# Kernel tuning notes

Hardware: AMD Instinct MI355X
Metric: run time of the kernel (lower is better)

The kernel has to match this reference:

```python
import jax, jax.numpy as jnp
import numpy as np

B, N, H, HEADS, L = 8, 64, 512, 8, 4
VOCAB, NBOND, CLS = 128, 8, 2
SP = H // HEADS
SCALE = float(np.sqrt(H))  # module divides by sqrt(hidden_dim), not sqrt(sp_dim)


def _ln(x):
    # fresh nn.LayerNorm each call -> gamma=1, beta=0
    m = jnp.mean(x, -1, keepdims=True)
    v = jnp.mean((x - m) ** 2, -1, keepdims=True)
    return (x - m) / jnp.sqrt(v + 1e-5)


def _split(x):  # [B,N,H] -> [B,h,N,sp]
    return x.reshape(B, N, HEADS, SP).transpose(0, 2, 1, 3)


def setup_inputs() -> dict:
    key = jax.random.key(0)
    ks = jax.random.split(key, 16)
    s = 0.05
    return {
        "input_batch": jax.random.randint(ks[0], (B, N), 0, VOCAB),
        "adj_m": jax.random.randint(ks[1], (B, N, N), 0, NBOND),
        "atom_emb": jax.random.normal(ks[2], (VOCAB, H), jnp.float32) * s,
        "bond_emb": jax.random.normal(ks[3], (NBOND, H), jnp.float32) * s,
        "Wq": jax.random.normal(ks[4], (L, H, H), jnp.float32) * s,
        "Wk": jax.random.normal(ks[5], (L, H, H), jnp.float32) * s,
        "Wv": jax.random.normal(ks[6], (L, H, H), jnp.float32) * s,
        "Wew": jax.random.normal(ks[7], (L, H, H), jnp.float32) * s,
        "Wstack": jax.random.normal(ks[8], (L, H, H), jnp.float32) * s,
        "Wf1": jax.random.normal(ks[9], (L, H, 4 * H), jnp.float32) * s,
        "Wf2": jax.random.normal(ks[10], (L, 4 * H, H), jnp.float32) * s,
        "Wout": jax.random.normal(ks[11], (H, H), jnp.float32) * s,
        "Wpred": jax.random.normal(ks[12], (H, CLS), jnp.float32) * s,
        "bpred": jnp.zeros((CLS,), jnp.float32),
    }


def _forward(input_batch, adj_m, atom_emb, bond_emb, Wq, Wk, Wv, Wew,
             Wstack, Wf1, Wf2, Wout, Wpred, bpred):
    x = atom_emb[input_batch]        # [B,N,H] atom embeddings
    bond = bond_emb[adj_m]           # [B,N,N,H] bond embeddings
    neg = jnp.where(adj_m > 0, 0.0, -jnp.inf)[:, None, :, :]  # [B,1,N,N]
    for l in range(L):
        xn = _ln(x)
        q = _split(xn @ Wq[l])
        k = _split(xn @ Wk[l])
        v = _split(xn @ Wv[l])
        ew = bond @ Wew[l]           # [B,N,N,H]
        w = ew.reshape(B, N, N, HEADS, SP).transpose(0, 3, 1, 2, 4)  # [B,h,N,N,sp]
        # bond_influence==1: sim_ij = q_i . (k_j + w_ij)
        logits = jnp.einsum('bhid,bhjd->bhij', q, k) \
               + jnp.einsum('bhid,bhijd->bhij', q, w)
        attn = jax.nn.softmax(logits / SCALE + neg, axis=-1)
        o = jnp.einsum('bhij,bhjd->bhid', attn, v)
        o = o.transpose(0, 2, 1, 3).reshape(B, N, H) @ Wstack[l]
        attn_resid = o + xn
        ff = jax.nn.relu(_ln(attn_resid) @ Wf1[l]) @ Wf2[l]
        x = ff + attn_resid          # transformer_output
        # edge attention update: softmax over {w.w, w.x_i, w.x_j}
        ew_s = jnp.sum(ew * ew, -1)                      # [B,N,N]
        a0 = jnp.einsum('bijh,bih->bij', ew, x)
        a1 = jnp.einsum('bijh,bjh->bij', ew, x)
        wgt = jax.nn.softmax(jnp.stack([ew_s, a0, a1], -1) / SCALE, -1)  # [B,N,N,3]
        bond = (wgt[..., 0:1] * ew
                + wgt[..., 1:2] * x[:, :, None, :]
                + wgt[..., 2:3] * x[:, None, :, :])      # new edge state
    cls = jnp.tanh(x[:, 0, :] @ Wout)
    return jax.nn.softmax(cls @ Wpred + bpred, axis=-1)


def reference(input_batch, adj_m, atom_emb, bond_emb, Wq, Wk, Wv, Wew,
              Wstack, Wf1, Wf2, Wout, Wpred, bpred):
    return _forward(input_batch, adj_m, atom_emb, bond_emb, Wq, Wk, Wv, Wew,
                    Wstack, Wf1, Wf2, Wout, Wpred, bpred)
```

## Files before the change

### kernel.cpp

```cpp
#include <hip/hip_runtime.h>
#include <hip/hip_bf16.h>

typedef __hip_bfloat16 bf16;

#define B_     8
#define N_     64
#define H_     512
#define HEADS_ 8
#define SP_    64
#define L_     4
static constexpr float INV_SCALE = 0.044194173824159216f;

typedef __attribute__((ext_vector_type(8))) short short8;
typedef __attribute__((ext_vector_type(4))) float f32x4;

__device__ __forceinline__ void unpack8(uint4 u, float* f) {
    f[0] = __uint_as_float(u.x << 16); f[1] = __uint_as_float(u.x & 0xffff0000u);
    f[2] = __uint_as_float(u.y << 16); f[3] = __uint_as_float(u.y & 0xffff0000u);
    f[4] = __uint_as_float(u.z << 16); f[5] = __uint_as_float(u.z & 0xffff0000u);
    f[6] = __uint_as_float(u.w << 16); f[7] = __uint_as_float(u.w & 0xffff0000u);
}

__device__ __forceinline__ bf16 f2bf(float v) { return __float2bfloat16(v); }

// ... 28 lines not shown
    const int cE = cA * 8;

    for (int k0 = kbeg; k0 < kend; k0 += 64) {
        uint4 a0 = *(const uint4*)(A  + (size_t)(bm + rA) * K + k0 + cE);
        uint4 a1 = *(const uint4*)(A  + (size_t)(bm + rA + 32) * K + k0 + cE);
        uint4 b0 = *(const uint4*)(Bt + (size_t)(bn + rA) * K + k0 + cE);
        uint4 b1 = *(const uint4*)(Bt + (size_t)(bn + rA + 32) * K + k0 + cE);
        __syncthreads();
        *(uint4*)(As + ksP * (64 * RSTR) + rA * RSTR + cB) = a0;
        *(uint4*)(As + ksP * (64 * RSTR) + (rA + 32) * RSTR + cB) = a1;
        *(uint4*)(Bs + ksP * (64 * RSTR) + rA * RSTR + cB) = b0;
        *(uint4*)(Bs + ksP * (64 * RSTR) + (rA + 32) * RSTR + cB) = b1;
        __syncthreads();
        short8 af[2][2], bfr[2][2];
        #pragma unroll
        for (int ks = 0; ks < 2; ++ks)
            #pragma unroll
            for (int t = 0; t < 2; ++t) {
                af[ks][t]  = *(const short8*)(As + ks * (64 * RSTR) + (wr + t * 16 + m0) * RSTR + q4 * 16);
                bfr[ks][t] = *(const short8*)(Bs + ks * (64 * RSTR) + (wc + t * 16 + m0) * RSTR + q4 * 16);
            }
        #pragma unroll
        for (int ks = 0; ks < 2; ++ks)
            #pragma unroll
            for (int mt = 0; mt < 2; ++mt)
                #pragma unroll
                for (int nt = 0; nt < 2; ++nt)
                    acc[mt][nt] = __builtin_amdgcn_mfma_f32_16x16x32_bf16(
                        af[ks][mt], bfr[ks][nt], acc[mt][nt], 0, 0, 0);
    }

    if (EPI <= 1) {
        float* C = (float*)Cv;
        #pragma unroll
        for (int mt = 0; mt < 2; ++mt)
            #pragma unroll
            for (int i = 0; i < 4; ++i) {
                int row = bm + wr + mt * 16 + q4 * 4 + i;
                #pragma unroll
                for (int nt = 0; nt < 2; ++nt) {
                    int col = bn + wc + nt * 16 + m0;
                    float v = acc[mt][nt][i];
                    if (EPI == 1) v += R[(size_t)row * N + col];
                    C[(size_t)row * N + col] = v;
                }
            }
    } else {
        bf16* C = (bf16*)Cv;
        #pragma unroll
        for (int mt = 0; mt < 2; ++mt)
            #pragma unroll
            for (int i = 0; i < 4; ++i) {
                int row = bm + wr + mt * 16 + q4 * 4 + i;
                #pragma unroll
                for (int nt = 0; nt < 2; ++nt) {
                    int col = bn + wc + nt * 16 + m0;
                    float v = acc[mt][nt][i];
                    if (EPI == 2) v = fmaxf(v, 0.0f);
                    C[(size_t)row * N + col] = __float2bfloat16(v);
                }
            }
    }
}

template <int EPI, bool SPLIT>
__launch_bounds__(256)
__global__ void mfma_gemm_s(const bf16* __restrict__ A, const bf16* __restrict__ Bt,
                            void* __restrict__ Cv, const float* __restrict__ R,
                            int M, int N, int K) {
    __shared__ __align__(16) char lds[4 * 64 * RSTR];
    int kbeg = 0, kend = K;
    const bf16* B2 = Bt;
    void* C2 = Cv;
    if (SPLIT) {
        int ks = K / gridDim.z;
        kbeg = blockIdx.z * ks;
        kend = kbeg + ks;
        C2 = (void*)((float*)Cv + (size_t)blockIdx.z * M * N);
        gemm64_body<0>(lds, A, B2, C2, nullptr, M, N, K, blockIdx.x, blockIdx.y, kbeg, kend);
    } else {
        B2 = Bt + (size_t)blockIdx.z * N * K;
        if (EPI <= 1) C2 = (void*)((float*)Cv + (size_t)blockIdx.z * M * N);
        gemm64_body<EPI>(lds, A, B2, C2, R, M, N, K, blockIdx.x, blockIdx.y, kbeg, kend);
    }
}


__device__ __forceinline__ void ptable_body(char* lds, const float* __restrict__ q,
        const bf16* __restrict__ Bt, float* __restrict__ P, int b, int h, bool shr) {
    char* As = lds;
    char* Bs = lds + 2 * 64 * RSTR;
    const int tid = threadIdx.x;
    const int w = tid >> 6, lane = tid & 63;
    const int wr = (w >> 1) * 32, wc = (w & 1) * 32;
    const int m0 = lane & 15, q4 = lane >> 4;
    const int rA = tid >> 3;
    const int cA = tid & 7;
    const int ksP = cA >> 2;
    const int cB = (cA & 3) * 16;
    const int cE = cA * 8;

    const float* Aq = q + (size_t)(b * 64) * 512 + h * 64;
    const bf16*  Bb = Bt + (shr ? (size_t)0 : (size_t)b * 64 * 512) + h * 64;

    float4 fa0 = *(const float4*)(Aq + (size_t)rA * 512 + cE);
    float4 fa1 = *(const float4*)(Aq + (size_t)rA * 512 + cE + 4);
    float4 fb0 = *(const float4*)(Aq + (size_t)(rA + 32) * 512 + cE);
    float4 fb1 = *(const float4*)(Aq + (size_t)(rA + 32) * 512 + cE + 4);
    uint4 bv0 = *(const uint4*)(Bb + (size_t)rA * 512 + cE);
    uint4 bv1 = *(const uint4*)(Bb + (size_t)(rA + 32) * 512 + cE);
    uint4 av0 = pack8bf(fa0, fa1);
    uint4 av1 = pack8bf(fb0, fb1);
    *(uint4*)(As + ksP * (64 * RSTR) + rA * RSTR + cB) = av0;
    *(uint4*)(As + ksP * (64 * RSTR) + (rA + 32) * RSTR + cB) = av1;
    *(uint4*)(Bs + ksP * (64 * RSTR) + rA * RSTR + cB) = bv0;
    *(uint4*)(Bs + ksP * (64 * RSTR) + (rA + 32) * RSTR + cB) = bv1;
    __syncthreads();

    f32x4 acc[2][2] = {};
    short8 af[2][2], bfr[2][2];
    #pragma unroll
    for (int ks = 0; ks < 2; ++ks)
        #pragma unroll
        for (int t = 0; t < 2; ++t) {
            af[ks][t]  = *(const short8*)(As + ks * (64 * RSTR) + (wr + t * 16 + m0) * RSTR + q4 * 16);
            bfr[ks][t] = *(const short8*)(Bs + ks * (64 * RSTR) + (wc + t * 16 + m0) * RSTR + q4 * 16);
        }
    #pragma unroll
    for (int ks = 0; ks < 2; ++ks)
        #pragma unroll
        for (int mt = 0; mt < 2; ++mt)
            #pragma unroll
            for (int nt = 0; nt < 2; ++nt)
                acc[mt][nt] = __builtin_amdgcn_mfma_f32_16x16x32_bf16(
                    af[ks][mt], bfr[ks][nt], acc[mt][nt], 0, 0, 0);

    #pragma unroll
    for (int mt = 0; mt < 2; ++mt)
        #pragma unroll
        for (int i = 0; i < 4; ++i) {
            int row = wr + mt * 16 + q4 * 4 + i;
            #pragma unroll
            for (int nt = 0; nt < 2; ++nt) {
                int col = wc + nt * 16 + m0;
                P[(((size_t)b * 8 + h) * 64 + row) * 64 + col] = acc[mt][nt][i];
            }
        }
}

__device__ __forceinline__ void ugemm_body(char* lds, const float* __restrict__ q,
        const bf16* __restrict__ wc3, bf16* __restrict__ ubf, int h, int mb, int nb) {
    char* As = lds;
    char* Bs = lds + 2 * 64 * RSTR;
    const int tid = threadIdx.x;
    const int w = tid >> 6, lane = tid & 63;
    const int wr = (w >> 1) * 32, wc = (w & 1) * 32;
    const int m0 = lane & 15, q4 = lane >> 4;
    const int rA = tid >> 3;
    const int cA = tid & 7;
    const int ksP = cA >> 2;
    const int cB = (cA & 3) * 16;
    const int cE = cA * 8;

    const float* Aq = q + (size_t)(mb * 64) * 512 + h * 64;
    const bf16*  Bt = wc3 + (size_t)(nb * 64) * 512 + h * 64;

// ... 41 lines not shown
            }
        }
}

__device__ __forceinline__ void coeff1_body(const int* __restrict__ adj,
        const float* __restrict__ c0a, const float* __restrict__ c1a, const float* __restrict__ c2a,
        const float* __restrict__ gbuf, int row, int j,
        float* __restrict__ w0o, float* __restrict__ w1o, float* __restrict__ w2o) {
    int b = row >> 6, i = row & 63;
    int p = row * 64 + j;
    int t = adj[p];
    const float* TXX = gbuf + 0 * 32768 + (size_t)b * 4096;
    const float* TEX = gbuf + 1 * 32768 + (size_t)b * 4096;
    const float* TXx = gbuf + 2 * 32768 + (size_t)b * 4096;
    const float* TEx = gbuf + 3 * 32768 + (size_t)b * 4096;
    const float* TEE = gbuf + 4 * 32768 + (size_t)b * 4096;
    float c0 = c0a[p], c1 = c1a[p], c2 = c2a[p];
    float s1 = c0 * TEx[t * 64 + i] + c1 * TXx[i * 64 + i] + c2 * TXx[j * 64 + i];
    float s2 = c0 * TEx[t * 64 + j] + c1 * TXx[i * 64 + j] + c2 * TXx[j * 64 + j];
    float s0 = c0 * c0 * TEE[t * 64 + t] + c1 * c1 * TXX[i * 64 + i] + c2 * c2 * TXX[j * 64 + j]
             + 2.f * c0 * c1 * TEX[t * 64 + i] + 2.f * c0 * c2 * TEX[t * 64 + j]
             + 2.f * c1 * c2 * TXX[i * 64 + j];
    float t0 = s0 * INV_SCALE, t1 = s1 * INV_SCALE, t2 = s2 * INV_SCALE;
    float m = fmaxf(t0, fmaxf(t1, t2));
    float e0 = expf(t0 - m), e1 = expf(t1 - m), e2 = expf(t2 - m);
    float inv = 1.0f / (e0 + e1 + e2);
    w0o[p] = e0 * inv;
    w1o[p] = e1 * inv;
    w2o[p] = e2 * inv;
}

__device__ __forceinline__ void coeff2_body(const int* __restrict__ adj,
        const float* __restrict__ c0a, const float* __restrict__ c1a, const float* __restrict__ c2a,
        const float* __restrict__ c0b, const float* __restrict__ c1b, const float* __restrict__ c2b,
        const float* __restrict__ gbuf, int row, int j,
        float* __restrict__ w0o, float* __restrict__ w1o, float* __restrict__ w2o) {
    int b = row >> 6, i = row & 63;
    int p = row * 64 + j;
    int t = adj[p];
    const float* TXX = gbuf + 0 * 32768 + (size_t)b * 4096;
    const float* TXY = gbuf + 1 * 32768 + (size_t)b * 4096;
    const float* TYY = gbuf + 2 * 32768 + (size_t)b * 4096;
    const float* TEX = gbuf + 3 * 32768 + (size_t)b * 4096;
    const float* TEY = gbuf + 4 * 32768 + (size_t)b * 4096;
    const float* TEE = gbuf + 5 * 32768 + (size_t)b * 4096;
    const float* TXx = gbuf + 6 * 32768 + (size_t)b * 4096;
    const float* TYx = gbuf + 7 * 32768 + (size_t)b * 4096;
    const float* TEx = gbuf + 8 * 32768 + (size_t)b * 4096;
    float a0 = c0b[p];
    float AE = a0 * c0a[p], Aa = a0 * c1a[p], Ab = a0 * c2a[p];
    float Ac = c1b[p], Ad = c2b[p];
    float s1 = AE * TEx[t * 64 + i] + Aa * TXx[i * 64 + i] + Ab * TXx[j * 64 + i]
             + Ac * TYx[i * 64 + i] + Ad * TYx[j * 64 + i];
    float s2 = AE * TEx[t * 64 + j] + Aa * TXx[i * 64 + j] + Ab * TXx[j * 64 + j]
             + Ac * TYx[i * 64 + j] + Ad * TYx[j * 64 + j];
    float s0 = AE * AE * TEE[t * 64 + t] + Aa * Aa * TXX[i * 64 + i] + Ab * Ab * TXX[j * 64 + j]
             + Ac * Ac * TYY[i * 64 + i] + Ad * Ad * TYY[j * 64 + j]
             + 2.f * AE * Aa * TEX[t * 64 + i] + 2.f * AE * Ab * TEX[t * 64 + j]
             + 2.f * AE * Ac * TEY[t * 64 + i] + 2.f * AE * Ad * TEY[t * 64 + j]
             + 2.f * Aa * Ab * TXX[i * 64 + j]
             + 2.f * Aa * Ac * TXY[i * 64 + i] + 2.f * Aa * Ad * TXY[i * 64 + j]
             + 2.f * Ab * Ac * TXY[j * 64 + i] + 2.f * Ab * Ad * TXY[j * 64 + j]
             + 2.f * Ac * Ad * TYY[i * 64 + j];
    float t0 = s0 * INV_SCALE, t1 = s1 * INV_SCALE, t2 = s2 * INV_SCALE;
    float m = fmaxf(t0, fmaxf(t1, t2));
    float e0 = expf(t0 - m), e1 = expf(t1 - m), e2 = expf(t2 - m);
    float inv = 1.0f / (e0 + e1 + e2);
    w0o[p] = e0 * inv;
    w1o[p] = e1 * inv;
    w2o[p] = e2 * inv;
}

__launch_bounds__(256)
__global__ void setup_kernel(const int* __restrict__ ids, const float* __restrict__ atom_emb,
                             const float* __restrict__ bond_emb,
                             const float* __restrict__ Wq, const float* __restrict__ Wk,
                             const float* __restrict__ Wv, const float* __restrict__ Wew,
                             const float* __restrict__ Wst,
                             const float* __restrict__ Wf1, const float* __restrict__ Wf2,
                             float* __restrict__ xn, bf16* __restrict__ xn_bf,
                             bf16* __restrict__ qkvt, bf16* __restrict__ ewt,
                             bf16* __restrict__ stackt,
                             bf16* __restrict__ f1t, bf16* __restrict__ f2t,
                             bf16* __restrict__ bond_bf, bf16* __restrict__ wc3) {
    __shared__ __align__(16) float smem[64 * 65];
    const size_t KN = (size_t)H_ * H_;
    int bid = blockIdx.x;
    int tid = threadIdx.x;

    if (bid < 512) {
        int row = bid;
        const float* r = atom_emb + (size_t)ids[row] * H_;
        float x0 = r[tid], x1 = r[tid + 256];
        float s = x0 + x1, sq = x0 * x0 + x1 * x1;
        #pragma unroll
        for (int off = 32; off; off >>= 1) {
            s  += __shfl_xor(s,  off);
            sq += __shfl_xor(sq, off);
        }
        int w = tid >> 6;
        if ((tid & 63) == 0) { smem[w] = s; smem[4 + w] = sq; }
        __syncthreads();
        float S = smem[0] + smem[1] + smem[2] + smem[3];
        float Q = smem[4] + smem[5] + smem[6] + smem[7];
        float mean = S * (1.0f / H_);
        float var  = Q * (1.0f / H_) - mean * mean;
        float inv  = rsqrtf(var + 1e-5f);
        float y0 = (x0 - mean) * inv, y1 = (x1 - mean) * inv;
        xn[(size_t)row * H_ + tid]       = y0;
        xn[(size_t)row * H_ + tid + 256] = y1;
        xn_bf[(size_t)row * H_ + tid]       = f2bf(y0);
        xn_bf[(size_t)row * H_ + tid + 256] = f2bf(y1);
    } else if (bid < 3840) {
        const float* W; bf16* Wt; int K, N, kb, nb;
        if (bid < 1792) {
            int idx = bid - 512;
            int z = idx >> 6, rem = idx & 63;
            kb = rem & 7; nb = rem >> 3;
            K = 512; N = 512;
            if (z < 12) {
                int sss = z >> 2, l = z & 3;
                W  = (sss == 0 ? Wq : sss == 1 ? Wk : Wv) + (size_t)l * KN;
                Wt = qkvt + (size_t)l * 3 * KN + (size_t)sss * KN;
            } else if (z < 16) {
                int l = z - 12;
                W = Wew + (size_t)l * KN; Wt = ewt + (size_t)l * KN;
            } else {
                int l = z - 16;
                W = Wst + (size_t)l * KN; Wt = stackt + (size_t)l * KN;
            }
        } else {
            int idx = bid - 1792;
            int z = idx >> 8;
            int idx2 = idx & 255;
            const size_t KN4 = (size_t)4 * H_ * H_;
            if (z < 4) {
                W = Wf1 + (size_t)z * KN4; Wt = f1t + (size_t)z * KN4; K = 512; N = 2048;
                kb = idx2 & 7; nb = idx2 >> 3;
            } else {
                W = Wf2 + (size_t)(z - 4) * KN4; Wt = f2t + (size_t)(z - 4) * KN4; K = 2048; N = 512;
                kb = idx2 >> 3; nb = idx2 & 7;
            }
        }
        int k0 = kb * 64, n0 = nb * 64;
        float (*tt)[65] = (float(*)[65])smem;
        int rr = tid >> 4, c4 = (tid & 15) * 4;
        #pragma unroll
        for (int it = 0; it < 4; ++it) {
            float4 v = *(const float4*)(W + (size_t)(k0 + rr + it * 16) * N + n0 + c4);
            tt[rr + it * 16][c4 + 0] = v.x;
            tt[rr + it * 16][c4 + 1] = v.y;
            tt[rr + it * 16][c4 + 2] = v.z;
            tt[rr + it * 16][c4 + 3] = v.w;
        }
        __syncthreads();
        int nr = tid >> 3, k8 = (tid & 7) * 8;
        #pragma unroll
        for (int it = 0; it < 2; ++it) {
            int nn = nr + it * 32;
            __align__(16) bf16 ob[8];
            #pragma unroll
            for (int e = 0; e < 8; ++e)
                ob[e] = f2bf(tt[k8 + e][nn]);
            *(uint4*)(Wt + (size_t)(n0 + nn) * K + k0 + k8) = *(const uint4*)ob;
        }
    } else if (bid < 3968) {
        int idx = bid - 3840;
        int t = idx >> 1;
        int c = (idx & 1) * 256 + tid;
        bond_bf[t * 512 + c] = (t < 8) ? f2bf(bond_emb[t * 512 + c]) : f2bf(0.0f);
    } else {
        int idx = bid - 3968;
        int gid = idx * 256 + tid;
// ... 171 lines not shown
    ptable_body(lds, q, Bt, P, b, h, z == 1);
}

__launch_bounds__(256)
__global__ void l3qkv_g2(const bf16* __restrict__ xn_bf, const bf16* __restrict__ qkvt_l,
                         float* __restrict__ qkv,
                         const bf16* __restrict__ xw12, const bf16* __restrict__ x2w2,
                         const bf16* __restrict__ e0w12, const bf16* __restrict__ x_bf,
                         float* __restrict__ gbuf) {
    __shared__ __align__(16) char lds[4 * 64 * RSTR];
    int bid = blockIdx.x;
    if (bid < 192) {
        int z = bid >> 6, rem = bid & 63;
        int mb = rem >> 3, by = rem & 7;
        gemm64_body<0>(lds, xn_bf, qkvt_l + (size_t)z * 262144,
                       qkv + (size_t)z * 262144, nullptr, 512, 512, 512, mb, by, 0, 512);
    } else {
        int k = bid - 192;
        int b = k & 7, z = k >> 3;
        size_t ob = (size_t)b * 32768;
        const bf16 *A, *Bt;
        switch (z) {
            case 0: A = xw12 + ob; Bt = xw12 + ob; break;
            case 1: A = xw12 + ob; Bt = x2w2 + ob; break;
            case 2: A = x2w2 + ob; Bt = x2w2 + ob; break;
            case 3: A = e0w12;     Bt = xw12 + ob; break;
            case 4: A = e0w12;     Bt = x2w2 + ob; break;
            case 5: A = e0w12;     Bt = e0w12;     break;
            case 6: A = xw12 + ob; Bt = x_bf + ob; break;
            case 7: A = x2w2 + ob; Bt = x_bf + ob; break;
            default: A = e0w12;    Bt = x_bf + ob; break;
        }
        float* C = gbuf + (size_t)z * 32768 + (size_t)b * 4096;
        gemm64_body<0>(lds, A, Bt, C, nullptr, 64, 64, 512, 0, 0, 0, 512);
    }
}

__launch_bounds__(256)
__global__ void u_c2(const float* __restrict__ q, const bf16* __restrict__ wc3,
                     bf16* __restrict__ ubf,
                     const int* __restrict__ adj,
                     const float* __restrict__ c0a, const float* __restrict__ c1a,
                     const float* __restrict__ c2a,
                     const float* __restrict__ c0b, const float* __restrict__ c1b,
                     const float* __restrict__ c2b,
                     const float* __restrict__ gbuf,
                     float* __restrict__ w0o, float* __restrict__ w1o,
                     float* __restrict__ w2o) {
    __shared__ __align__(16) char lds[4 * 64 * RSTR];
    int bid = blockIdx.x;
    if (bid < 512) {
        int h = bid >> 6, mb = (bid >> 3) & 7, nb = bid & 7;
        ugemm_body(lds, q, wc3, ubf, h, mb, nb);
    } else {
        int k = bid - 512;
        int tid = threadIdx.x;
        int j = tid & 63;
        #pragma unroll
        for (int pass = 0; pass < 2; ++pass) {
            int row = k * 8 + pass * 4 + (tid >> 6);
            coeff2_body(adj, c0a, c1a, c2a, c0b, c1b, c2b, gbuf, row, j, w0o, w1o, w2o);
        }
    }
}

__launch_bounds__(256)
__global__ void mbuf_gemm(const bf16* __restrict__ ubf, const bf16* __restrict__ xw12,
                          const bf16* __restrict__ x2w2, const bf16* __restrict__ x_bf,
                          const bf16* __restrict__ e0w12,
                          float* __restrict__ MX, float* __restrict__ MY,
                          float* __restrict__ MZ, float* __restrict__ DE) {
    __shared__ __align__(16) char lds[4 * 64 * RSTR];
    int b = blockIdx.x, mt = blockIdx.y, z = blockIdx.z;
    const bf16* A = ubf + (size_t)b * 512 * 512;
    const bf16* Bt;
    float* C;
    if (z == 0)      { Bt = xw12 + (size_t)b * 64 * 512; C = MX + (size_t)b * 512 * 64; }
    else if (z == 1) { Bt = x2w2 + (size_t)b * 64 * 512; C = MY + (size_t)b * 512 * 64; }
    else if (z == 2) { Bt = x_bf + (size_t)b * 64 * 512; C = MZ + (size_t)b * 512 * 64; }
    else             { Bt = e0w12;                        C = DE + (size_t)b * 512 * 64; }
    gemm64_body<0>(lds, A, Bt, C, nullptr, 512, 64, 512, mt, 0, 0, 512);
}

__global__ void reduce_stack_ln(const float* __restrict__ part, const float* __restrict__ base,
                                float* __restrict__ resid, bf16* __restrict__ ffin_bf) {
    const int MN = 512 * H_;
    int row = blockIdx.x;
    int tid = threadIdx.x;
    size_t b0 = (size_t)row * H_;
    float v0 = base[b0 + tid], v1 = base[b0 + tid + 256];
    #pragma unroll
    for (int s = 0; s < 4; ++s) {
        v0 += part[(size_t)s * MN + b0 + tid];
        v1 += part[(size_t)s * MN + b0 + tid + 256];
    }
    resid[b0 + tid] = v0;
    resid[b0 + tid + 256] = v1;
    float s = v0 + v1, sq = v0 * v0 + v1 * v1;
    #pragma unroll
    for (int off = 32; off; off >>= 1) {
        s  += __shfl_xor(s,  off);
        sq += __shfl_xor(sq, off);
    }
    __shared__ float ls[4], lq[4];
    int w = tid >> 6;
    if ((tid & 63) == 0) { ls[w] = s; lq[w] = sq; }
    __syncthreads();
    float S = ls[0] + ls[1] + ls[2] + ls[3];
    float Q = lq[0] + lq[1] + lq[2] + lq[3];
    float mean = S * (1.0f / H_);
    float var  = Q * (1.0f / H_) - mean * mean;
    float inv  = rsqrtf(var + 1e-5f);
    ffin_bf[b0 + tid]       = f2bf((v0 - mean) * inv);
    ffin_bf[b0 + tid + 256] = f2bf((v1 - mean) * inv);
}

template <bool DO_LN>
__global__ void reduce_ln_kernel(const float* __restrict__ part, const float* __restrict__ resid,
                                 float* __restrict__ x, bf16* __restrict__ x_bf,
                                 float* __restrict__ xn, bf16* __restrict__ xn_bf) {
    const int MN = 512 * H_;
    int row = blockIdx.x;
    int tid = threadIdx.x;
    size_t base = (size_t)row * H_;
    float v0 = resid[base + tid], v1 = resid[base + tid + 256];
    #pragma unroll
    for (int s = 0; s < 4; ++s) {
        v0 += part[(size_t)s * MN + base + tid];
        v1 += part[(size_t)s * MN + base + tid + 256];
    }
    x[base + tid] = v0;
    x[base + tid + 256] = v1;
    x_bf[base + tid]       = f2bf(v0);
    x_bf[base + tid + 256] = f2bf(v1);
    if (DO_LN) {
        float s = v0 + v1, sq = v0 * v0 + v1 * v1;
        #pragma unroll
        for (int off = 32; off; off >>= 1) {
            s  += __shfl_xor(s,  off);
            sq += __shfl_xor(sq, off);
        }
        __shared__ float ls[4], lq[4];
        int w = tid >> 6;
        if ((tid & 63) == 0) { ls[w] = s; lq[w] = sq; }
        __syncthreads();
        float S = ls[0] + ls[1] + ls[2] + ls[3];
        float Q = lq[0] + lq[1] + lq[2] + lq[3];
        float mean = S * (1.0f / H_);
        float var  = Q * (1.0f / H_) - mean * mean;
        float inv  = rsqrtf(var + 1e-5f);
        float y0 = (v0 - mean) * inv, y1 = (v1 - mean) * inv;
        xn[base + tid]       = y0;
        xn[base + tid + 256] = y1;
        xn_bf[base + tid]       = f2bf(y0);
        xn_bf[base + tid + 256] = f2bf(y1);
    }
}

template <bool GATHER>
__global__ void attn_kernel(const float* __restrict__ qkv, const bf16* __restrict__ ew,
                            const int* __restrict__ adj, bf16* __restrict__ o) {
    const float* q = qkv;
    const float* k = qkv + (size_t)512 * H_;
    const float* v = qkv + (size_t)1024 * H_;
    int bi = blockIdx.x;
    int b  = bi >> 6;
    int ty = threadIdx.y;
    int h  = blockIdx.y * 4 + ty;
    int lane = threadIdx.x;
    __shared__ float qs[4][64], as[4][64];
    qs[ty][lane] = q[(size_t)bi * H_ + h * 64 + lane];
    __syncthreads();

    int j = lane;
    int pair = bi * 64 + j;
    int aj = adj[pair];
    const float4* k4 = (const float4*)(k + (size_t)(b * 64 + j) * H_ + h * 64);
    const uint4*  w4 = (const uint4*)((GATHER ? ew + (size_t)aj * H_
                                              : ew + (size_t)pair * H_) + h * 64);
    float acc = 0.f;
    #pragma unroll
    for (int t = 0; t < 8; ++t) {
        uint4 wu = w4[t];
        float4 ka = k4[2 * t], kb = k4[2 * t + 1];
        float wf[8];
        unpack8(wu, wf);
        const float* qq = &qs[ty][t * 8];
        acc += qq[0] * (ka.x + wf[0]) + qq[1] * (ka.y + wf[1])
             + qq[2] * (ka.z + wf[2]) + qq[3] * (ka.w + wf[3])
             + qq[4] * (kb.x + wf[4]) + qq[5] * (kb.y + wf[5])
             + qq[6] * (kb.z + wf[6]) + qq[7] * (kb.w + wf[7]);
    }
    float logit = acc * INV_SCALE;
    if (aj <= 0) logit = -INFINITY;

    float m = logit;
    #pragma unroll
    for (int off = 32; off; off >>= 1) m = fmaxf(m, __shfl_xor(m, off));
    float p = expf(logit - m);
    float s = p;
    #pragma unroll
    for (int off = 32; off; off >>= 1) s += __shfl_xor(s, off);
    as[ty][lane] = p / s;
    __syncthreads();

    const float* vbase = v + (size_t)(b * 64) * H_ + h * 64;
    float oacc = 0.f;
    int d = lane;
    #pragma unroll 8
    for (int jj = 0; jj < 64; ++jj)
        oacc += as[ty][jj] * vbase[(size_t)jj * H_ + d];
    o[(size_t)bi * H_ + h * 64 + d] = __float2bfloat16(oacc);
}

template <int MODE>
__global__ void attn13_kernel(const float* __restrict__ qkv, const int* __restrict__ adj,
        const float* __restrict__ c0a, const float* __restrict__ c1a, const float* __restrict__ c2a,
        const float* __restrict__ c0b, const float* __restrict__ c1b, const float* __restrict__ c2b,
        const float* __restrict__ PX, const float* __restrict__ PY, const float* __restrict__ PE,
        bf16* __restrict__ o) {
    const float* q = qkv;
    const float* k = qkv + (size_t)512 * H_;
    const float* v = qkv + (size_t)1024 * H_;
    int bi = blockIdx.x;
    int b  = bi >> 6, i = bi & 63;
    int ty = threadIdx.y;
    int h  = blockIdx.y * 4 + ty;
    int lane = threadIdx.x;
    __shared__ float qs[4][64], as[4][64];
    qs[ty][lane] = q[(size_t)bi * H_ + h * 64 + lane];
    __syncthreads();

    int j = lane;
    int p = bi * 64 + j;
    int t = adj[p];
    size_t pb = (((size_t)b * 8 + h) * 64 + i) * 64;
    float acc;
    if (MODE == 1) {
        acc = c0a[p] * PE[pb + t] + c1a[p] * PX[pb + i] + c2a[p] * PX[pb + j];
    } else {
        float a0 = c0b[p];
// ... 14 lines not shown
    if (t <= 0) logit = -INFINITY;

    float m = logit;
    #pragma unroll
    for (int off = 32; off; off >>= 1) m = fmaxf(m, __shfl_xor(m, off));
    float pe = expf(logit - m);
    float s = pe;
    #pragma unroll
    for (int off = 32; off; off >>= 1) s += __shfl_xor(s, off);
    as[ty][lane] = pe / s;
    __syncthreads();

    const float* vbase = v + (size_t)(b * 64) * H_ + h * 64;
    float oacc = 0.f;
    int d = lane;
    #pragma unroll 8
    for (int jj = 0; jj < 64; ++jj)
        oacc += as[ty][jj] * vbase[(size_t)jj * H_ + d];
    o[(size_t)bi * H_ + h * 64 + d] = __float2bfloat16(oacc);
}

__global__ void attn3s2_kernel(const float* __restrict__ qkv, const int* __restrict__ adj,
        const float* __restrict__ c0a, const float* __restrict__ c1a, const float* __restrict__ c2a,
        const float* __restrict__ c0b, const float* __restrict__ c1b, const float* __restrict__ c2b,
        const float* __restrict__ v0c, const float* __restrict__ v1c, const float* __restrict__ v2c,
        const float* __restrict__ MX, const float* __restrict__ MY,
        const float* __restrict__ MZ, const float* __restrict__ DE,
        bf16* __restrict__ o) {
    const float* q = qkv;
    const float* k = qkv + (size_t)512 * H_;
    const float* v = qkv + (size_t)1024 * H_;
    int bi = blockIdx.x;
    int b  = bi >> 6, i = bi & 63;
    int ty = threadIdx.y;
    int h  = blockIdx.y * 4 + ty;
    int lane = threadIdx.x;
    __shared__ float qs[4][64], as[4][64];
    qs[ty][lane] = q[(size_t)bi * H_ + h * 64 + lane];
    __syncthreads();

    int j = lane;
    int p = bi * 64 + j;
    int t = adj[p];
    float v0 = v0c[p];
    float q0 = v0 * c0b[p];
    float AE = q0 * c0a[p], Aa = q0 * c1a[p], Ab = q0 * c2a[p];
    float Ac = v0 * c1b[p], Ad = v0 * c2b[p];
    float Ae = v1c[p], Af = v2c[p];
    size_t rb = ((size_t)b * 512 + i * 8 + h) * 64;
    float acc = AE * DE[rb + t]
              + Aa * MX[rb + i] + Ac * MY[rb + i] + Ae * MZ[rb + i]
              + Ab * MX[rb + j] + Ad * MY[rb + j] + Af * MZ[rb + j];

    const float4* k4 = (const float4*)(k + (size_t)(b * 64 + j) * H_ + h * 64);
    #pragma unroll
    for (int tt = 0; tt < 8; ++tt) {
        float4 ka = k4[2 * tt], kb = k4[2 * tt + 1];
        const float* qq = &qs[ty][tt * 8];
        acc += qq[0] * ka.x + qq[1] * ka.y + qq[2] * ka.z + qq[3] * ka.w
             + qq[4] * kb.x + qq[5] * kb.y + qq[6] * kb.z + qq[7] * kb.w;
    }
    float logit = acc * INV_SCALE;
    if (t <= 0) logit = -INFINITY;

    float m = logit;
    #pragma unroll
    for (int off = 32; off; off >>= 1) m = fmaxf(m, __shfl_xor(m, off));
    float pe = expf(logit - m);
    float s = pe;
    #pragma unroll
    for (int off = 32; off; off >>= 1) s += __shfl_xor(s, off);
    as[ty][lane] = pe / s;
    __syncthreads();

    const float* vbase = v + (size_t)(b * 64) * H_ + h * 64;
    float oacc = 0.f;
    int d = lane;
    #pragma unroll 8
    for (int jj = 0; jj < 64; ++jj)
        oacc += as[ty][jj] * vbase[(size_t)jj * H_ + d];
    o[(size_t)bi * H_ + h * 64 + d] = __float2bfloat16(oacc);
}

__global__ void cls_part_kernel(const float* __restrict__ x, const float* __restrict__ Wout,
                                float* __restrict__ clspart) {
    int b  = blockIdx.x;
    int cb = blockIdx.y;
    int ks = blockIdx.z;
    int tid = threadIdx.x;
    int c  = cb * 64 + (tid & 63);
    int kk = tid >> 6;
    const float* xr = x + (size_t)(b * 64) * H_;
    int h0 = ks * 128 + kk * 32;
    float acc = 0.f;
    #pragma unroll
    for (int h = 0; h < 32; ++h)
        acc += xr[h0 + h] * Wout[(size_t)(h0 + h) * H_ + c];
    __shared__ float red[4][64];
    red[kk][tid & 63] = acc;
    __syncthreads();
    if (tid < 64) {
        float v = red[0][tid] + red[1][tid] + red[2][tid] + red[3][tid];
        clspart[((size_t)ks * 8 + b) * H_ + cb * 64 + tid] = v;
    }
}

__global__ void cls_pred2_kernel(const float* __restrict__ clspart,
                                 const float* __restrict__ Wpred,
                                 const float* __restrict__ bpred,
                                 float* __restrict__ out) {
    int b = blockIdx.x;
    int tid = threadIdx.x;
    __shared__ float red0[4], red1[4];
    float a0 = 0.f, a1 = 0.f;
    #pragma unroll
    for (int t = 0; t < 2; ++t) {
        int c = tid + t * 256;
        float v = clspart[((size_t)0 * 8 + b) * H_ + c]
                + clspart[((size_t)1 * 8 + b) * H_ + c]
                + clspart[((size_t)2 * 8 + b) * H_ + c]
                + clspart[((size_t)3 * 8 + b) * H_ + c];
        float tv = tanhf(v);
        a0 += tv * Wpred[c * 2 + 0];
        a1 += tv * Wpred[c * 2 + 1];
    }
    #pragma unroll
    for (int off = 32; off; off >>= 1) {
        a0 += __shfl_xor(a0, off);
        a1 += __shfl_xor(a1, off);
    }
    int w = tid >> 6;
    if ((tid & 63) == 0) { red0[w] = a0; red1[w] = a1; }
    __syncthreads();
    if (tid == 0) {
        float s0 = red0[0] + red0[1] + red0[2] + red0[3] + bpred[0];
        float s1 = red1[0] + red1[1] + red1[2] + red1[3] + bpred[1];
        float m = fmaxf(s0, s1);
        float e0 = expf(s0 - m), e1 = expf(s1 - m);
        float inv = 1.0f / (e0 + e1);
        out[b * 2 + 0] = e0 * inv;
        out[b * 2 + 1] = e1 * inv;
    }
}

extern "C" void kernel_launch(void* const* d_in, const int* in_sizes, int n_in,
                              void* d_out, int out_size, void* d_ws, size_t ws_size,
                              hipStream_t stream) {
    const int*   ids      = (const int*)d_in[0];
    const int*   adj      = (const int*)d_in[1];
    const float* atom_emb = (const float*)d_in[2];
    const float* bond_emb = (const float*)d_in[3];
    const float* Wq     = (const float*)d_in[4];
    const float* Wk     = (const float*)d_in[5];
    const float* Wv     = (const float*)d_in[6];
    const float* Wew    = (const float*)d_in[7];
    const float* Wstack = (const float*)d_in[8];
    const float* Wf1    = (const float*)d_in[9];
    const float* Wf2    = (const float*)d_in[10];
    const float* Wout   = (const float*)d_in[11];
    const float* Wpred  = (const float*)d_in[12];
    const float* bpred  = (const float*)d_in[13];

    char* ws = (char*)d_ws;
    size_t off = 0;
    auto alloc = [&](size_t bytes) {
        size_t o = off;
        off += (bytes + 255) & ~(size_t)255;
        return o;
    };
    const size_t ROWS  = (size_t)B_ * N_;
    const size_t PAIRS = (size_t)B_ * N_ * N_;
    const size_t KN    = (size_t)H_ * H_;

    float* x       = (float*)(ws + alloc(ROWS * H_ * 4));
    float* xn      = (float*)(ws + alloc(ROWS * H_ * 4));
    bf16*  xn_bf   = (bf16*) (ws + alloc(ROWS * H_ * 2));
    bf16*  x_bf    = (bf16*) (ws + alloc(ROWS * H_ * 2));
    float* qkv     = (float*)(ws + alloc(3 * ROWS * H_ * 4));
    bf16*  o_bf    = (bf16*) (ws + alloc(ROWS * H_ * 2));
    float* resid   = (float*)(ws + alloc(ROWS * H_ * 4));
    bf16*  ffin_bf = (bf16*) (ws + alloc(ROWS * H_ * 2));
    bf16*  ffh_bf  = (bf16*) (ws + alloc(ROWS * 4 * H_ * 2));
    float* part    = (float*)(ws + alloc(4 * ROWS * H_ * 4));
    float* clspart = (float*)(ws + alloc(4 * 8 * H_ * 4));
    bf16*  ubf     = (bf16*) (ws + alloc(ROWS * 8 * 512 * 2));
    float* MX      = (float*)(ws + alloc((size_t)4096 * 64 * 4));
    float* MY      = (float*)(ws + alloc((size_t)4096 * 64 * 4));
    float* MZ      = (float*)(ws + alloc((size_t)4096 * 64 * 4));
    float* DE      = (float*)(ws + alloc((size_t)4096 * 64 * 4));
    float* PT0     = (float*)(ws + alloc((size_t)4096 * 64 * 4));
    float* PT1     = (float*)(ws + alloc((size_t)4096 * 64 * 4));
    float* PT2     = (float*)(ws + alloc((size_t)4096 * 64 * 4));
    float* gbuf    = (float*)(ws + alloc((size_t)9 * 8 * 4096 * 4));
    bf16*  wc3     = (bf16*) (ws + alloc(KN * 2));
    bf16*  bond_bf = (bf16*) (ws + alloc(64 * H_ * 2));
    bf16*  E0      = (bf16*) (ws + alloc(64 * H_ * 2));
    bf16*  e0w1    = (bf16*) (ws + alloc(64 * H_ * 2));
    bf16*  e0w12   = (bf16*) (ws + alloc(64 * H_ * 2));
    bf16*  xw1     = (bf16*) (ws + alloc(KN * 2));
    bf16*  xw12    = (bf16*) (ws + alloc(KN * 2));
    bf16*  x2w2    = (bf16*) (ws + alloc(KN * 2));
    float* cw      = (float*)(ws + alloc(9 * PAIRS * 4));
    bf16*  qkvt    = (bf16*) (ws + alloc((size_t)L_ * 3 * KN * 2));
    bf16*  ewt     = (bf16*) (ws + alloc((size_t)L_ * KN * 2));
    bf16*  stackt  = (bf16*) (ws + alloc((size_t)L_ * KN * 2));
    bf16*  f1t     = (bf16*) (ws + alloc((size_t)L_ * 4 * KN * 2));
    bf16*  f2t     = (bf16*) (ws + alloc((size_t)L_ * 4 * KN * 2));
    (void)ws_size;

    float* cw0a = cw;
    float* cw1a = cw + PAIRS;
    float* cw2a = cw + 2 * PAIRS;
    float* cw0b = cw + 3 * PAIRS;
    float* cw1b = cw + 4 * PAIRS;
    float* cw2b = cw + 5 * PAIRS;
    float* cw0c = cw + 6 * PAIRS;
    float* cw1c = cw + 7 * PAIRS;
    float* cw2c = cw + 8 * PAIRS;

    setup_kernel<<<4096, 256, 0, stream>>>(ids, atom_emb, bond_emb,
                                           Wq, Wk, Wv, Wew, Wstack, Wf1, Wf2,
                                           xn, xn_bf, qkvt, ewt, stackt, f1t, f2t,
                                           bond_bf, wc3);

    for (int l = 0; l < L_; ++l) {
        if (l == 0) {
            qkv0_e0<<<200, 256, 0, stream>>>(xn_bf, qkvt, qkv, bond_bf, ewt, E0);
            attn_kernel<true><<<dim3(512, 2), dim3(64, 4), 0, stream>>>(qkv, E0, adj, o_bf);
        } else if (l == 1) {
            basis1_qkv_ec<<<2312, 256, 0, stream>>>(
                x_bf, E0, ewt + KN, xw1, e0w1, xn_bf, qkvt + (size_t)3 * KN, qkv,
                adj, x, cw0a, cw1a, cw2a);
            ptable_kernel<<<dim3(8, 8, 2), 256, 0, stream>>>(qkv, xw1, e0w1, PT0, PT1);
            attn13_kernel<1><<<dim3(512, 2), dim3(64, 4), 0, stream>>>(
                qkv, adj, cw0a, cw1a, cw2a, nullptr, nullptr, nullptr,
                PT0, nullptr, PT1, o_bf);
        } else if (l == 2) {
            basis2_qkv_g1<<<368, 256, 0, stream>>>(
                xw1, x_bf, e0w1, ewt + 2 * KN, xw12, x2w2, e0w12,
                xn_bf, qkvt + (size_t)6 * KN, qkv, gbuf);
            ptable2c<<<256, 256, 0, stream>>>(
                qkv, xw12, x2w2, e0w12, PT0, PT1, PT2,
                adj, cw0a, cw1a, cw2a, gbuf, cw0b, cw1b, cw2b);
            attn13_kernel<2><<<dim3(512, 2), dim3(64, 4), 0, stream>>>(
                qkv, adj, cw0a, cw1a, cw2a, cw0b, cw1b, cw2b,
                PT0, PT1, PT2, o_bf);
        } else {
            l3qkv_g2<<<264, 256, 0, stream>>>(
                xn_bf, qkvt + (size_t)9 * KN, qkv, xw12, x2w2, e0w12, x_bf, gbuf);
            u_c2<<<576, 256, 0, stream>>>(
                qkv, wc3, ubf, adj, cw0a, cw1a, cw2a, cw0b, cw1b, cw2b,
                gbuf, cw0c, cw1c, cw2c);
            mbuf_gemm<<<dim3(8, 8, 4), 256, 0, stream>>>(ubf, xw12, x2w2, x_bf, e0w12,
                                                         MX, MY, MZ, DE);
            attn3s2_kernel<<<dim3(512, 2), dim3(64, 4), 0, stream>>>(
                qkv, adj, cw0a, cw1a, cw2a, cw0b, cw1b, cw2b, cw0c, cw1c, cw2c,
                MX, MY, MZ, DE, o_bf);
        }

        mfma_gemm_s<0, true><<<dim3(8, 8, 4), 256, 0, stream>>>(
            o_bf, stackt + (size_t)l * KN, part, nullptr, 512, 512, 512);
        reduce_stack_ln<<<512, 256, 0, stream>>>(part, xn, resid, ffin_bf);
        mfma_gemm_s<2, false><<<dim3(8, 32), 256, 0, stream>>>(
            ffin_bf, f1t + (size_t)l * 4 * KN, ffh_bf, nullptr, 512, 2048, 512);
        mfma_gemm_s<0, true><<<dim3(8, 8, 4), 256, 0, stream>>>(
            ffh_bf, f2t + (size_t)l * 4 * KN, part, nullptr, 512, 512, 2048);
        if (l < L_ - 1)
            reduce_ln_kernel<true><<<512, 256, 0, stream>>>(part, resid, x, x_bf, xn, xn_bf);
        else
            reduce_ln_kernel<false><<<512, 256, 0, stream>>>(part, resid, x, x_bf, xn, xn_bf);
    }

    cls_part_kernel<<<dim3(8, 8, 4), 256, 0, stream>>>(x, Wout, clspart);
    cls_pred2_kernel<<<8, 256, 0, stream>>>(clspart, Wpred, bpred, (float*)d_out);
}
```

Before: 345.9 us.

## Fuse split-K reductions and LayerNorm into GEMM tails via last-block atomic counters

The split-K Wstack and Wf2 GEMMs now do their own reduction and LayerNorm. An atomic counter per 64-row stripe picks the last block to finish, and that block sums the four partials and applies the residual and LN, so the separate reduce kernels are gone. The two classifier kernels are merged the same way, with one last block computing the tanh, pred and softmax. This removes about nine kernel launches and their launch gaps, at the cost of serialising the reduction of each stripe onto a single block and adding fence and atomic overhead.

Result: slower. 691.1 us (+99.8%).

```diff
diff --git a/kernel.cpp b/kernel.cpp
--- a/kernel.cpp
+++ b/kernel.cpp
@@ -134,6 +134,108 @@
         B2 = Bt + (size_t)blockIdx.z * N * K;
         if (EPI <= 1) C2 = (void*)((float*)Cv + (size_t)blockIdx.z * M * N);
         gemm64_body<EPI>(lds, A, B2, C2, R, M, N, K, blockIdx.x, blockIdx.y, kbeg, kend);
+    }
+}
+
+__launch_bounds__(256)
+__global__ void stackred_kernel(const bf16* __restrict__ o_bf, const bf16* __restrict__ stackt_l,
+                                float* __restrict__ part, const float* __restrict__ xn,
+                                float* __restrict__ resid, bf16* __restrict__ ffin_bf,
+                                int* __restrict__ cnt) {
+    __shared__ __align__(16) char lds[4 * 64 * RSTR];
+    __shared__ int lastf;
+    int bid = blockIdx.x;
+    int bz = bid >> 6, rem = bid & 63, bx = rem >> 3, by = rem & 7;
+    gemm64_body<0>(lds, o_bf, stackt_l, part + (size_t)bz * 262144, nullptr,
+                   512, 512, 512, bx, by, bz * 128, bz * 128 + 128);
+    __threadfence();
+    __syncthreads();
+    if (threadIdx.x == 0) lastf = (atomicAdd(&cnt[bx], 1) == 31);
+    __syncthreads();
+    if (!lastf) return;
+    __threadfence();
+    const int MN = 512 * 512;
+    int wv = threadIdx.x >> 6, lane = threadIdx.x & 63;
+    for (int k = 0; k < 16; ++k) {
+        int r = bx * 64 + wv * 16 + k;
+        size_t rb = (size_t)r * 512;
+        float vals[8], s = 0.f, sq = 0.f;
+        #pragma unroll
+        for (int e = 0; e < 8; ++e) {
+            int col = lane + e * 64;
+            float v = xn[rb + col] + part[0 * MN + rb + col] + part[1 * MN + rb + col]
+                    + part[2 * MN + rb + col] + part[3 * MN + rb + col];
+            vals[e] = v; s += v; sq += v * v;
+            resid[rb + col] = v;
+        }
+        #pragma unroll
+        for (int off = 32; off; off >>= 1) {
+            s  += __shfl_xor(s,  off);
+            sq += __shfl_xor(sq, off);
+        }
+        float mean = s * (1.0f / H_);
+        float var  = sq * (1.0f / H_) - mean * mean;
+        float inv  = rsqrtf(var + 1e-5f);
+        #pragma unroll
+        for (int e = 0; e < 8; ++e) {
+            int col = lane + e * 64;
+            ffin_bf[rb + col] = f2bf((vals[e] - mean) * inv);
+        }
+    }
+}
+
+template <bool DO_LN>
+__launch_bounds__(256)
+__global__ void ff2red_kernel(const bf16* __restrict__ ffh_bf, const bf16* __restrict__ f2t_l,
+                              float* __restrict__ part, const float* __restrict__ resid,
+                              float* __restrict__ x, bf16* __restrict__ x_bf,
+                              float* __restrict__ xn, bf16* __restrict__ xn_bf,
+                              int* __restrict__ cnt) {
+    __shared__ __align__(16) char lds[4 * 64 * RSTR];
+    __shared__ int lastf;
+    int bid = blockIdx.x;
+    int bz = bid >> 6, rem = bid & 63, bx = rem >> 3, by = rem & 7;
+    gemm64_body<0>(lds, ffh_bf, f2t_l, part + (size_t)bz * 262144, nullptr,
+                   512, 512, 2048, bx, by, bz * 512, bz * 512 + 512);
+    __threadfence();
+    __syncthreads();
+    if (threadIdx.x == 0) lastf = (atomicAdd(&cnt[bx], 1) == 31);
+    __syncthreads();
+    if (!lastf) return;
+    __threadfence();
+    const int MN = 512 * 512;
+    int wv = threadIdx.x >> 6, lane = threadIdx.x & 63;
+    for (int k = 0; k < 16; ++k) {
+        int r = bx * 64 + wv * 16 + k;
+        size_t rb = (size_t)r * 512;
+        float vals[8], s = 0.f, sq = 0.f;
+        #pragma unroll
+        for (int e = 0; e < 8; ++e) {
+            int col = lane + e * 64;
+            float v = resid[rb + col] + part[0 * MN + rb + col] + part[1 * MN + rb + col]
+                    + part[2 * MN + rb + col] + part[3 * MN + rb + col];
+            vals[e] = v;
+            if (DO_LN) { s += v; sq += v * v; }
+            x[rb + col] = v;
+            x_bf[rb + col] = f2bf(v);
+        }
+        if (DO_LN) {
+            #pragma unroll
+            for (int off = 32; off; off >>= 1) {
+                s  += __shfl_xor(s,  off);
+                sq += __shfl_xor(sq, off);
+            }
+            float mean = s * (1.0f / H_);
+            float var  = sq * (1.0f / H_) - mean * mean;
+            float inv  = rsqrtf(var + 1e-5f);
+            #pragma unroll
+            for (int e = 0; e < 8; ++e) {
+                int col = lane + e * 64;
+                float y = (vals[e] - mean) * inv;
+                xn[rb + col] = y;
+                xn_bf[rb + col] = f2bf(y);
+            }
+        }
     }
 }
 
@@ -341,13 +443,15 @@
                              bf16* __restrict__ qkvt, bf16* __restrict__ ewt,
                              bf16* __restrict__ stackt,
                              bf16* __restrict__ f1t, bf16* __restrict__ f2t,
-                             bf16* __restrict__ bond_bf, bf16* __restrict__ wc3) {
+                             bf16* __restrict__ bond_bf, bf16* __restrict__ wc3,
+                             int* __restrict__ cnt) {
     __shared__ __align__(16) float smem[64 * 65];
     const size_t KN = (size_t)H_ * H_;
     int bid = blockIdx.x;
     int tid = threadIdx.x;
 
     if (bid < 512) {
+        if (bid == 0 && tid < 72) cnt[tid] = 0;
         int row = bid;
         const float* r = atom_emb + (size_t)ids[row] * H_;
         float x0 = r[tid], x1 = r[tid + 256];
@@ -685,81 +789,6 @@
     gemm64_body<0>(lds, A, Bt, C, nullptr, 512, 64, 512, mt, 0, 0, 512);
 }
 
-__global__ void reduce_stack_ln(const float* __restrict__ part, const float* __restrict__ base,
-                                float* __restrict__ resid, bf16* __restrict__ ffin_bf) {
-    const int MN = 512 * H_;
-    int row = blockIdx.x;
-    int tid = threadIdx.x;
-    size_t b0 = (size_t)row * H_;
-    float v0 = base[b0 + tid], v1 = base[b0 + tid + 256];
-    #pragma unroll
-    for (int s = 0; s < 4; ++s) {
-        v0 += part[(size_t)s * MN + b0 + tid];
-        v1 += part[(size_t)s * MN + b0 + tid + 256];
-    }
-    resid[b0 + tid] = v0;
-    resid[b0 + tid + 256] = v1;
-    float s = v0 + v1, sq = v0 * v0 + v1 * v1;
-    #pragma unroll
-    for (int off = 32; off; off >>= 1) {
-        s  += __shfl_xor(s,  off);
-        sq += __shfl_xor(sq, off);
-    }
-    __shared__ float ls[4], lq[4];
-    int w = tid >> 6;
-    if ((tid & 63) == 0) { ls[w] = s; lq[w] = sq; }
-    __syncthreads();
-    float S = ls[0] + ls[1] + ls[2] + ls[3];
-    float Q = lq[0] + lq[1] + lq[2] + lq[3];
-    float mean = S * (1.0f / H_);
-    float var  = Q * (1.0f / H_) - mean * mean;
-    float inv  = rsqrtf(var + 1e-5f);
-    ffin_bf[b0 + tid]       = f2bf((v0 - mean) * inv);
-    ffin_bf[b0 + tid + 256] = f2bf((v1 - mean) * inv);
-}
-
-template <bool DO_LN>
-__global__ void reduce_ln_kernel(const float* __restrict__ part, const float* __restrict__ resid,
-                                 float* __restrict__ x, bf16* __restrict__ x_bf,
-                                 float* __restrict__ xn, bf16* __restrict__ xn_bf) {
-    const int MN = 512 * H_;
-    int row = blockIdx.x;
-    int tid = threadIdx.x;
-    size_t base = (size_t)row * H_;
-    float v0 = resid[base + tid], v1 = resid[base + tid + 256];
-    #pragma unroll
-    for (int s = 0; s < 4; ++s) {
-        v0 += part[(size_t)s * MN + base + tid];
-        v1 += part[(size_t)s * MN + base + tid + 256];
-    }
-    x[base + tid] = v0;
-    x[base + tid + 256] = v1;
-    x_bf[base + tid]       = f2bf(v0);
-    x_bf[base + tid + 256] = f2bf(v1);
-    if (DO_LN) {
-        float s = v0 + v1, sq = v0 * v0 + v1 * v1;
-        #pragma unroll
-        for (int off = 32; off; off >>= 1) {
-            s  += __shfl_xor(s,  off);
-            sq += __shfl_xor(sq, off);
-        }
-        __shared__ float ls[4], lq[4];
-        int w = tid >> 6;
-        if ((tid & 63) == 0) { ls[w] = s; lq[w] = sq; }
-        __syncthreads();
-        float S = ls[0] + ls[1] + ls[2] + ls[3];
-        float Q = lq[0] + lq[1] + lq[2] + lq[3];
-        float mean = S * (1.0f / H_);
-        float var  = Q * (1.0f / H_) - mean * mean;
-        float inv  = rsqrtf(var + 1e-5f);
-        float y0 = (v0 - mean) * inv, y1 = (v1 - mean) * inv;
-        xn[base + tid]       = y0;
-        xn[base + tid + 256] = y1;
-        xn_bf[base + tid]       = f2bf(y0);
-        xn_bf[base + tid + 256] = f2bf(y1);
-    }
-}
-
 template <bool GATHER>
 __global__ void attn_kernel(const float* __restrict__ qkv, const bf16* __restrict__ ew,
                             const int* __restrict__ adj, bf16* __restrict__ o) {
@@ -940,11 +969,13 @@
     o[(size_t)bi * H_ + h * 64 + d] = __float2bfloat16(oacc);
 }
 
-__global__ void cls_part_kernel(const float* __restrict__ x, const float* __restrict__ Wout,
-                                float* __restrict__ clspart) {
-    int b  = blockIdx.x;
-    int cb = blockIdx.y;
-    int ks = blockIdx.z;
+__launch_bounds__(256)
+__global__ void cls_kernel(const float* __restrict__ x, const float* __restrict__ Wout,
+                           float* __restrict__ clspart,
+                           const float* __restrict__ Wpred, const float* __restrict__ bpred,
+                           float* __restrict__ out, int* __restrict__ cnt) {
+    int bid = blockIdx.x;
+    int ks = bid & 3, cb = (bid >> 2) & 7, b = bid >> 5;
     int tid = threadIdx.x;
     int c  = cb * 64 + (tid & 63);
     int kk = tid >> 6;
@@ -961,43 +992,46 @@
         float v = red[0][tid] + red[1][tid] + red[2][tid] + red[3][tid];
         clspart[((size_t)ks * 8 + b) * H_ + cb * 64 + tid] = v;
     }
-}
-
-__global__ void cls_pred2_kernel(const float* __restrict__ clspart,
-                                 const float* __restrict__ Wpred,
-                                 const float* __restrict__ bpred,
-                                 float* __restrict__ out) {
-    int b = blockIdx.x;
-    int tid = threadIdx.x;
+    __threadfence();
+    __syncthreads();
+    __shared__ int lastf;
+    if (tid == 0) lastf = (atomicAdd(&cnt[0], 1) == 255);
+    __syncthreads();
+    if (!lastf) return;
+    __threadfence();
+
     __shared__ float red0[4], red1[4];
-    float a0 = 0.f, a1 = 0.f;
-    #pragma unroll
-    for (int t = 0; t < 2; ++t) {
-        int c = tid + t * 256;
-        float v = clspart[((size_t)0 * 8 + b) * H_ + c]
-                + clspart[((size_t)1 * 8 + b) * H_ + c]
-                + clspart[((size_t)2 * 8 + b) * H_ + c]
-                + clspart[((size_t)3 * 8 + b) * H_ + c];
-        float tv = tanhf(v);
-        a0 += tv * Wpred[c * 2 + 0];
-        a1 += tv * Wpred[c * 2 + 1];
-    }
-    #pragma unroll
-    for (int off = 32; off; off >>= 1) {
-        a0 += __shfl_xor(a0, off);
-        a1 += __shfl_xor(a1, off);
-    }
-    int w = tid >> 6;
-    if ((tid & 63) == 0) { red0[w] = a0; red1[w] = a1; }
-    __syncthreads();
-    if (tid == 0) {
-        float s0 = red0[0] + red0[1] + red0[2] + red0[3] + bpred[0];
-        float s1 = red1[0] + red1[1] + red1[2] + red1[3] + bpred[1];
-        float m = fmaxf(s0, s1);
-        float e0 = expf(s0 - m), e1 = expf(s1 - m);
-        float inv = 1.0f / (e0 + e1);
-        out[b * 2 + 0] = e0 * inv;
-        out[b * 2 + 1] = e1 * inv;
+    for (int bb = 0; bb < 8; ++bb) {
+        float a0 = 0.f, a1 = 0.f;
+        #pragma unroll
+        for (int t = 0; t < 2; ++t) {
+            int c2 = tid + t * 256;
+            float v = clspart[((size_t)0 * 8 + bb) * H_ + c2]
+                    + clspart[((size_t)1 * 8 + bb) * H_ + c2]
+                    + clspart[((size_t)2 * 8 + bb) * H_ + c2]
+                    + clspart[((size_t)3 * 8 + bb) * H_ + c2];
+            float tv = tanhf(v);
+            a0 += tv * Wpred[c2 * 2 + 0];
+            a1 += tv * Wpred[c2 * 2 + 1];
+        }
+        #pragma unroll
+        for (int off = 32; off; off >>= 1) {
+            a0 += __shfl_xor(a0, off);
+            a1 += __shfl_xor(a1, off);
+        }
+        int w = tid >> 6;
+        if ((tid & 63) == 0) { red0[w] = a0; red1[w] = a1; }
+        __syncthreads();
+        if (tid == 0) {
+            float s0 = red0[0] + red0[1] + red0[2] + red0[3] + bpred[0];
+            float s1 = red1[0] + red1[1] + red1[2] + red1[3] + bpred[1];
+            float m = fmaxf(s0, s1);
+            float e0 = expf(s0 - m), e1 = expf(s1 - m);
+            float inv = 1.0f / (e0 + e1);
+            out[bb * 2 + 0] = e0 * inv;
+            out[bb * 2 + 1] = e1 * inv;
+        }
+        __syncthreads();
     }
 }
 
@@ -1059,6 +1093,7 @@
     bf16*  xw12    = (bf16*) (ws + alloc(KN * 2));
     bf16*  x2w2    = (bf16*) (ws + alloc(KN * 2));
     float* cw      = (float*)(ws + alloc(9 * PAIRS * 4));
+    int*   cnt     = (int*)  (ws + alloc(72 * 4));
     bf16*  qkvt    = (bf16*) (ws + alloc((size_t)L_ * 3 * KN * 2));
     bf16*  ewt     = (bf16*) (ws + alloc((size_t)L_ * KN * 2));
     bf16*  stackt  = (bf16*) (ws + alloc((size_t)L_ * KN * 2));
@@ -1079,7 +1114,7 @@
     setup_kernel<<<4096, 256, 0, stream>>>(ids, atom_emb, bond_emb,
                                            Wq, Wk, Wv, Wew, Wstack, Wf1, Wf2,
                                            xn, xn_bf, qkvt, ewt, stackt, f1t, f2t,
-                                           bond_bf, wc3);
+                                           bond_bf, wc3, cnt);
 
     for (int l = 0; l < L_; ++l) {
         if (l == 0) {
@@ -1116,19 +1151,20 @@
                 MX, MY, MZ, DE, o_bf);
         }
 
-        mfma_gemm_s<0, true><<<dim3(8, 8, 4), 256, 0, stream>>>(
-            o_bf, stackt + (size_t)l * KN, part, nullptr, 512, 512, 512);
-        reduce_stack_ln<<<512, 256, 0, stream>>>(part, xn, resid, ffin_bf);
+        stackred_kernel<<<256, 256, 0, stream>>>(
+            o_bf, stackt + (size_t)l * KN, part, xn, resid, ffin_bf, cnt + l * 8);
         mfma_gemm_s<2, false><<<dim3(8, 32), 256, 0, stream>>>(
             ffin_bf, f1t + (size_t)l * 4 * KN, ffh_bf, nullptr, 512, 2048, 512);
-        mfma_gemm_s<0, true><<<dim3(8, 8, 4), 256, 0, stream>>>(
-            ffh_bf, f2t + (size_t)l * 4 * KN, part, nullptr, 512, 512, 2048);
         if (l < L_ - 1)
-            reduce_ln_kernel<true><<<512, 256, 0, stream>>>(part, resid, x, x_bf, xn, xn_bf);
+            ff2red_kernel<true><<<256, 256, 0, stream>>>(
+                ffh_bf, f2t + (size_t)l * 4 * KN, part, resid, x, x_bf, xn, xn_bf,
+                cnt + 32 + l * 8);
         else
-            reduce_ln_kernel<false><<<512, 256, 0, stream>>>(part, resid, x, x_bf, xn, xn_bf);
-    }
-
-    cls_part_kernel<<<dim3(8, 8, 4), 256, 0, stream>>>(x, Wout, clspart);
-    cls_pred2_kernel<<<8, 256, 0, stream>>>(clspart, Wpred, bpred, (float*)d_out);
-}
+            ff2red_kernel<false><<<256, 256, 0, stream>>>(
+                ffh_bf, f2t + (size_t)l * 4 * KN, part, resid, x, x_bf, xn, xn_bf,
+                cnt + 32 + l * 8);
+    }
+
+    cls_kernel<<<256, 256, 0, stream>>>(x, Wout, clspart, Wpred, bpred,
+                                        (float*)d_out, cnt + 64);
+}
```
